# Optimization experiments

Measured on AMD Instinct MI355X. Metric: run time of the kernel, lower is better.

## Reference

```python
import jax, jax.numpy as jnp
import numpy as np

K = 20  # neighbors


def knn_idx(x, k):
    # x: [B, C, N]; returns indices of k nearest neighbors (incl. self): [B, N, k]
    xx = jnp.sum(x * x, axis=1)                          # [B, N]
    inner = jnp.einsum('bcn,bcm->bnm', x, x)             # [B, N, N]
    pd = 2.0 * inner - xx[:, :, None] - xx[:, None, :]   # -squared distance
    _, idx = jax.lax.top_k(pd, k)                        # [B, N, k]
    return idx


def graph_feature(x, k):
    # x: [B, C, N] -> edge features [B, 2C, N, k]
    idx = knn_idx(x, k)                                  # [B, N, k]
    xt = jnp.swapaxes(x, 1, 2)                           # [B, N, C]
    nbr = jax.vmap(lambda f, i: f[i])(xt, idx)           # [B, N, k, C]
    ctr = xt[:, :, None, :]                              # [B, N, 1, C]
    feat = jnp.concatenate(
        [nbr - ctr, jnp.broadcast_to(ctr, nbr.shape)], axis=-1)  # [B, N, k, 2C]
    return jnp.transpose(feat, (0, 3, 1, 2))             # [B, 2C, N, k]


def blk2(x, w, s, t):
    # 1x1 Conv2d (no bias) + folded BN + LeakyReLU(0.2); x: [B, C, N, k]
    y = jnp.einsum('oc,bcnk->bonk', w, x)
    y = y * s[None, :, None, None] + t[None, :, None, None]
    return jax.nn.leaky_relu(y, 0.2)


def blk1(x, w, s, t):
    # 1x1 Conv1d (no bias) + folded BN + LeakyReLU(0.2); x: [B, C, N]
    y = jnp.einsum('oc,bcn->bon', w, x)
    y = y * s[None, :, None] + t[None, :, None]
    return jax.nn.leaky_relu(y, 0.2)


def setup_inputs() -> dict:
    key = jax.random.key(0)
    ks = jax.random.split(key, 32)
    inp = {'x': jax.random.normal(ks[0], (16, 2, 2048), jnp.float32)}
    wdims = [(64, 4), (64, 64), (64, 128), (64, 64), (64, 128),
             (1024, 192), (512, 1216), (256, 512), (1, 256)]
    for i, (o, c) in enumerate(wdims):
        inp[f'w{i+1}'] = jax.random.normal(ks[1 + i], (o, c), jnp.float32) * np.float32((2.0 / c) ** 0.5)
    bdims = [64, 64, 64, 64, 64, 1024, 512, 256]
    for i, d in enumerate(bdims):
        inp[f's{i+1}'] = jax.random.uniform(ks[10 + i], (d,), jnp.float32, 0.5, 1.5)
        inp[f't{i+1}'] = jax.random.normal(ks[18 + i], (d,), jnp.float32) * 0.1
    return inp


def reference(x, w1, w2, w3, w4, w5, w6, w7, w8, w9,
              s1, s2, s3, s4, s5, s6, s7, s8,
              t1, t2, t3, t4, t5, t6, t7, t8):
    B, _, N = x.shape
    h = graph_feature(x, K)                 # [B, 4, N, k]
    h = blk2(h, w1, s1, t1)
    h = blk2(h, w2, s2, t2)
    x1 = jnp.max(h, axis=-1)                # [B, 64, N]
    h = graph_feature(x1, K)                # [B, 128, N, k]
    h = blk2(h, w3, s3, t3)
    h = blk2(h, w4, s4, t4)
    x2 = jnp.max(h, axis=-1)                # [B, 64, N]
    h = graph_feature(x2, K)                # [B, 128, N, k]
    h = blk2(h, w5, s5, t5)
    x3 = jnp.max(h, axis=-1)                # [B, 64, N]
    cat = jnp.concatenate([x1, x2, x3], axis=1)   # [B, 192, N]
    e = blk1(cat, w6, s6, t6)               # [B, 1024, N]
    g = jnp.max(e, axis=-1, keepdims=True)  # global max [B, 1024, 1]
    g = jnp.broadcast_to(g, (B, g.shape[1], N))
    h = jnp.concatenate([g, x1, x2, x3], axis=1)  # [B, 1216, N]
    h = blk1(h, w7, s7, t7)
    h = blk1(h, w8, s8, t8)                 # dropout = identity (eval)
    y = jnp.einsum('oc,bcn->bon', w9, h)    # [B, 1, N]
    return jax.nn.sigmoid(y.reshape(B, -1))
```

## Files before the change

kernel.cpp:

```cpp
#include <hip/hip_runtime.h>
#include <math.h>

#define KNNK 20
#define BEFORE(v1, g1, v2, g2) (((v1) > (v2)) || ((v1) == (v2) && (g1) < (g2)))

typedef unsigned short u16;
typedef unsigned int u32;
typedef unsigned long long u64;
typedef __attribute__((ext_vector_type(8))) short short8v;
typedef __attribute__((ext_vector_type(4))) float f32x4;

__device__ __forceinline__ float lrelu(float v) { return v >= 0.f ? v : 0.2f * v; }

__device__ __forceinline__ u16 f2bf(float v) {
    u32 u = __float_as_uint(v);
    u += 0x7fffu + ((u >> 16) & 1u);
    return (u16)(u >> 16);
}
__device__ __forceinline__ float bf2f(u16 h) { return __uint_as_float(((u32)h) << 16); }

__device__ __forceinline__ u32 ordf(float v) {
    u32 u = __float_as_uint(v);
    return u ^ ((u32)((int)u >> 31) | 0x80000000u);
}
__device__ __forceinline__ u64 mkkey(float v, int g) {
    return ((u64)ordf(v) << 32) | (u32)(~(u32)g);
}

__device__ __forceinline__ void cvt8(const float* __restrict__ p, short8v& H8, short8v& M8, short8v& L8) {
    float4 a = *(const float4*)(p);
    float4 b4 = *(const float4*)(p + 4);
    float v[8] = {a.x, a.y, a.z, a.w, b4.x, b4.y, b4.z, b4.w};
    short8v H, M, L;
#pragma unroll
    for (int i = 0; i < 8; ++i) {
        float x = v[i];
        u16 h = f2bf(x);
        float r1 = x - bf2f(h);
        u16 m = f2bf(r1);
        float r2 = r1 - bf2f(m);
        H[i] = (short)h;
        M[i] = (short)m;
        L[i] = (short)f2bf(r2);
    }
    H8 = H; M8 = M; L8 = L;
}

__global__ __launch_bounds__(256) void xx_kernel(const float* __restrict__ f, long bstride, int C,
                                                 float* __restrict__ xx) {
    int i = blockIdx.x * 256 + threadIdx.x;
    int b = i >> 11, n = i & 2047;
    const float* fb = f + (long)b * bstride;
    float s = 0.f;
    for (int c = 0; c < C; ++c) { float v = fb[c * 2048 + n]; s = fmaf(v, v, s); }
    xx[i] = s;
}

__device__ __forceinline__ void topk_row(const float* __restrict__ srow, int lane, int* __restrict__ orow) {
    float b1 = -INFINITY, b2 = -INFINITY, b3 = -INFINITY;
    int j1 = 0, j2 = 0, j3 = 0;
#pragma unroll
    for (int j = 0; j < 32; ++j) {
        float vv = srow[lane + 64 * j];
        bool c1 = vv > b1;
        bool c2 = vv > b2;
        bool c3 = vv > b3;
        b3 = c2 ? b2 : (c3 ? vv : b3);
        j3 = c2 ? j2 : (c3 ? j : j3);
        b2 = c1 ? b1 : (c2 ? vv : b2);
        j2 = c1 ? j1 : (c2 ? j : j2);
        b1 = c1 ? vv : b1;
        j1 = c1 ? j : j1;
    }

    u64 ka = mkkey(b1, lane + (j1 << 6));
#pragma unroll
    for (int size = 2; size <= 64; size <<= 1) {
#pragma unroll
        for (int stride = size >> 1; stride >= 1; stride >>= 1) {
            u64 ok = __shfl_xor(ka, stride);
            bool low = (lane & stride) == 0;
            bool asc = (lane & size) == 0;
            bool f = ka > ok;
            bool take = (low == asc) ? f : !f;
            ka = take ? ka : ok;
        }
    }
    u64 w19 = __shfl(ka, 19);
    unsigned used = (1u << j1) | (1u << j2) | (1u << j3);
    u64 pend = mkkey(b2, lane + (j2 << 6));
    int pstate = 0;
    while (__any(pend > w19)) {
        u64 act = __ballot(pend > w19);
        int L = __ffsll((long long)act) - 1;
        u64 ck = __shfl(pend, L);
        u64 cfb = __ballot(lane < 20 && ck > ka);
        int p = 20 - __popcll(cfb);
        u64 up = __shfl_up(ka, 1);
        if (lane < 20) {
            if (lane > p) ka = up;
            else if (lane == p) ka = ck;
        }
        if (lane == L) {
            if (pstate == 0) {
                pend = mkkey(b3, lane + (j3 << 6));
                pstate = 1;
            } else {
                float nb = -INFINITY;
                int nj = 0;
#pragma unroll
                for (int j = 0; j < 32; ++j) {
                    float vvv = ((used >> j) & 1u) ? -INFINITY : srow[lane + 64 * j];
                    if (vvv > nb) { nb = vvv; nj = j; }
                }
                used |= 1u << nj;
                pend = mkkey(nb, lane + (nj << 6));
            }
        }
        w19 = __shfl(ka, 19);
    }
    if (lane < KNNK) orow[lane] = (int)(~(u32)ka) & 2047;
}

__global__ __launch_bounds__(512, 4) void knn_kernel(const float* __restrict__ f, long bstride, int C,
                                                     const float* __restrict__ xx, int* __restrict__ idx_out) {
    __shared__ __align__(16) float lds[8 * 2048];
    int b = blockIdx.y;
    int n0 = blockIdx.x * 8;
    int t = threadIdx.x;
    const float* fb = f + (long)b * bstride;

    for (int e = t; e < C * 8; e += 512) {
        int c = e >> 3, j = e & 7;
        lds[e] = fb[c * 2048 + n0 + j];
    }
    __syncthreads();

    float acc[8][4];
#pragma unroll
    for (int i = 0; i < 8; ++i)
#pragma unroll
        for (int j = 0; j < 4; ++j) acc[i][j] = 0.f;
    int m0 = t * 4;
    for (int c = 0; c < C; ++c) {
        float4 b4 = *(const float4*)(fb + c * 2048 + m0);
        float bv[4] = {b4.x, b4.y, b4.z, b4.w};
        float4 a0 = *(const float4*)(lds + c * 8);
        float4 a1 = *(const float4*)(lds + c * 8 + 4);
        float av[8] = {a0.x, a0.y, a0.z, a0.w, a1.x, a1.y, a1.z, a1.w};
#pragma unroll
        for (int i = 0; i < 8; ++i)
#pragma unroll
            for (int j = 0; j < 4; ++j) acc[i][j] = fmaf(av[i], bv[j], acc[i][j]);
    }
    float xn[8];
#pragma unroll
    for (int i = 0; i < 8; ++i) xn[i] = xx[b * 2048 + n0 + i];
    float4 xm4 = *(const float4*)(xx + b * 2048 + m0);
    float xm[4] = {xm4.x, xm4.y, xm4.z, xm4.w};

    __syncthreads();
#pragma unroll
    for (int i = 0; i < 8; ++i) {
        float4 o;
        o.x = (2.f * acc[i][0] - xn[i]) - xm[0];
        o.y = (2.f * acc[i][1] - xn[i]) - xm[1];
        o.z = (2.f * acc[i][2] - xn[i]) - xm[2];
        o.w = (2.f * acc[i][3] - xn[i]) - xm[3];
        *(float4*)(lds + i * 2048 + m0) = o;
    }
    __syncthreads();

    int wave = t >> 6, lane = t & 63;
    topk_row(lds + wave * 2048, lane, idx_out + ((long)b * 2048 + n0 + wave) * KNNK);
}

__global__ __launch_bounds__(256) void pq_kernel(const float* __restrict__ f, long bstride, int C,
                                                 const float* __restrict__ W, float* __restrict__ P,
                                                 float* __restrict__ Q) {
    __shared__ __align__(16) float wa[64 * 64];
    __shared__ __align__(16) float wq[64 * 64];
    __shared__ __align__(16) float X[64 * 64];
    int b = blockIdx.y, n0 = blockIdx.x * 64, t = threadIdx.x;
    const float* fb = f + (long)b * bstride;
    for (int e = t; e < C * 64; e += 256) {
        int k = e >> 6, c = e & 63;
        float a = W[c * 2 * C + k];
        float bv = W[c * 2 * C + C + k];
        wa[k * 64 + c] = a;
        wq[k * 64 + c] = bv - a;
    }
    for (int e = t; e < C * 64; e += 256) {
        int k = e >> 6, j = e & 63;
        X[e] = fb[k * 2048 + n0 + j];
    }
    __syncthreads();
    int cg = t >> 4, ng = t & 15;
    float accP[4][4] = {}, accQ[4][4] = {};
    for (int k = 0; k < C; ++k) {
        float4 a4 = *(const float4*)(wa + k * 64 + cg * 4);
        float4 q4 = *(const float4*)(wq + k * 64 + cg * 4);
        float4 x4 = *(const float4*)(X + k * 64 + ng * 4);
        float av[4] = {a4.x, a4.y, a4.z, a4.w};
        float qv[4] = {q4.x, q4.y, q4.z, q4.w};
        float xv[4] = {x4.x, x4.y, x4.z, x4.w};
#pragma unroll
        for (int i = 0; i < 4; ++i)
#pragma unroll
            for (int j = 0; j < 4; ++j) {
                accP[i][j] = fmaf(av[i], xv[j], accP[i][j]);
                accQ[i][j] = fmaf(qv[i], xv[j], accQ[i][j]);
            }
    }
#pragma unroll
    for (int j = 0; j < 4; ++j) {
        long n = n0 + ng * 4 + j;
        float4 pv = {accP[0][j], accP[1][j], accP[2][j], accP[3][j]};
        float4 qv = {accQ[0][j], accQ[1][j], accQ[2][j], accQ[3][j]};
        *(float4*)(P + ((long)b * 2048 + n) * 64 + cg * 4) = pv;
        *(float4*)(Q + ((long)b * 2048 + n) * 64 + cg * 4) = qv;
    }
}

__global__ __launch_bounds__(256) void splitw3_kernel(const float* __restrict__ W, u16* __restrict__ h,
                                                      u16* __restrict__ m, u16* __restrict__ l) {
    int i = blockIdx.x * 256 + threadIdx.x;
    float v = W[i];
    u16 hh = f2bf(v);
    float r1 = v - bf2f(hh);
    u16 mm = f2bf(r1);
    float r2 = r1 - bf2f(mm);
    h[i] = hh;
    m[i] = mm;
    l[i] = f2bf(r2);
}

__global__ __launch_bounds__(256) void edge2_mfma_kernel(
    const float* __restrict__ P, const float* __restrict__ Q, const int* __restrict__ idx,
    const u16* __restrict__ Wh, const u16* __restrict__ Wm, const u16* __restrict__ Wl,
    const float* __restrict__ sa, const float* __restrict__ ta, const float* __restrict__ sb,
    const float* __restrict__ tb, float* __restrict__ out, int cofs) {
    __shared__ __align__(16) float h1t[192 * 68];
    __shared__ int idxl[160];
    int b = blockIdx.y, n0 = blockIdx.x * 8, t = threadIdx.x;
    if (t < 160) idxl[t] = idx[((long)b * 2048 + n0) * KNNK + t];
    __syncthreads();

    for (int it = t; it < 2560; it += 256) {
        int col = it % 160, cg = it / 160;
        int p = col / 20;
        int j = idxl[col];
        int n = n0 + p;
        float4 pv = *(const float4*)(P + ((long)b * 2048 + j) * 64 + cg * 4);
        float4 qv = *(const float4*)(Q + ((long)b * 2048 + n) * 64 + cg * 4);
        float4 sv = *(const float4*)(sa + cg * 4);
        float4 tv = *(const float4*)(ta + cg * 4);
        float4 o;
        o.x = lrelu(fmaf(sv.x, pv.x + qv.x, tv.x));
        o.y = lrelu(fmaf(sv.y, pv.y + qv.y, tv.y));
        o.z = lrelu(fmaf(sv.z, pv.z + qv.z, tv.z));
        o.w = lrelu(fmaf(sv.w, pv.w + qv.w, tv.w));
        *(float4*)(h1t + col * 68 + cg * 4) = o;
    }
    for (int it = t; it < 512; it += 256) {
        int col = 160 + (it & 31), cg = it >> 5;
        float4 z = {0.f, 0.f, 0.f, 0.f};
        *(float4*)(h1t + col * 68 + cg * 4) = z;
    }
    __syncthreads();

    int wave = t >> 6, lane = t & 63, l15 = lane & 15, lq = lane >> 4;
    f32x4 acc[3][4];
#pragma unroll
    for (int ct = 0; ct < 3; ++ct)
#pragma unroll
        for (int mt = 0; mt < 4; ++mt) {
            f32x4 z = {0.f, 0.f, 0.f, 0.f};
            acc[ct][mt] = z;
        }

#pragma unroll
    for (int ct = 0; ct < 3; ++ct) {
        int col = (wave * 3 + ct) * 16 + l15;
        short8v bh[2], bm[2], bl[2];
#pragma unroll
        for (int kh = 0; kh < 2; ++kh) cvt8(h1t + col * 68 + kh * 32 + lq * 8, bh[kh], bm[kh], bl[kh]);
#pragma unroll
        for (int mt = 0; mt < 4; ++mt) {
#pragma unroll
            for (int kh = 0; kh < 2; ++kh) {
                int wo = (mt * 16 + l15) * 64 + kh * 32 + lq * 8;
                short8v ah = *(const short8v*)(Wh + wo);
                short8v am = *(const short8v*)(Wm + wo);
                short8v al = *(const short8v*)(Wl + wo);
                acc[ct][mt] = __builtin_amdgcn_mfma_f32_16x16x32_bf16(ah, bh[kh], acc[ct][mt], 0, 0, 0);
                acc[ct][mt] = __builtin_amdgcn_mfma_f32_16x16x32_bf16(ah, bm[kh], acc[ct][mt], 0, 0, 0);
                acc[ct][mt] = __builtin_amdgcn_mfma_f32_16x16x32_bf16(am, bh[kh], acc[ct][mt], 0, 0, 0);
                acc[ct][mt] = __builtin_amdgcn_mfma_f32_16x16x32_bf16(am, bm[kh], acc[ct][mt], 0, 0, 0);
                acc[ct][mt] = __builtin_amdgcn_mfma_f32_16x16x32_bf16(ah, bl[kh], acc[ct][mt], 0, 0, 0);
                acc[ct][mt] = __builtin_amdgcn_mfma_f32_16x16x32_bf16(al, bh[kh], acc[ct][mt], 0, 0, 0);
            }
        }
    }
    __syncthreads();

#pragma unroll
    for (int ct = 0; ct < 3; ++ct) {
        int col = (wave * 3 + ct) * 16 + l15;
#pragma unroll
        for (int mt = 0; mt < 4; ++mt) {
            float4 d = {acc[ct][mt][0], acc[ct][mt][1], acc[ct][mt][2], acc[ct][mt][3]};
            *(float4*)(h1t + col * 68 + mt * 16 + lq * 4) = d;
        }
    }
    __syncthreads();

    for (int id = t; id < 512; id += 256) {
        int co = id & 63, p = id >> 6;
        float sv = sb[co], tv = tb[co];
        float m = -INFINITY;
#pragma unroll 4
        for (int kk = 0; kk < KNNK; ++kk)
            m = fmaxf(m, lrelu(fmaf(sv, h1t[(p * 20 + kk) * 68 + co], tv)));
        out[(long)b * (192 * 2048) + (long)(cofs + co) * 2048 + n0 + p] = m;
    }
}

__global__ __launch_bounds__(256) void edge2_kernel(
    const float* __restrict__ P, const float* __restrict__ Q, const int* __restrict__ idx,
    const float* __restrict__ W2, const float* __restrict__ sa, const float* __restrict__ ta,
    const float* __restrict__ sb, const float* __restrict__ tb, float* __restrict__ out, int cofs) {
    __shared__ __align__(16) float h1[64 * 164];
    __shared__ __align__(16) float w2l[64 * 64];
    __shared__ int idxl[160];
    int b = blockIdx.y, n0 = blockIdx.x * 8, t = threadIdx.x;
    if (t < 160) idxl[t] = idx[((long)b * 2048 + n0) * KNNK + t];
    for (int e = t; e < 4096; e += 256) { int co = e >> 6, ci = e & 63; w2l[ci * 64 + co] = W2[e]; }
    __syncthreads();
    for (int it = t; it < 2560; it += 256) {
        int col = it % 160, cg = it / 160;
        int p = col / 20;
        int j = idxl[col];
        int n = n0 + p;
        float4 pv = *(const float4*)(P + ((long)b * 2048 + j) * 64 + cg * 4);
        float4 qv = *(const float4*)(Q + ((long)b * 2048 + n) * 64 + cg * 4);
        float4 sv = *(const float4*)(sa + cg * 4);
        float4 tv = *(const float4*)(ta + cg * 4);
        h1[(cg * 4 + 0) * 164 + col] = lrelu(fmaf(sv.x, pv.x + qv.x, tv.x));
        h1[(cg * 4 + 1) * 164 + col] = lrelu(fmaf(sv.y, pv.y + qv.y, tv.y));
        h1[(cg * 4 + 2) * 164 + col] = lrelu(fmaf(sv.z, pv.z + qv.z, tv.z));
        h1[(cg * 4 + 3) * 164 + col] = lrelu(fmaf(sv.w, pv.w + qv.w, tv.w));
    }
    __syncthreads();
    int p = t & 7, co2 = t >> 3, c0 = co2 * 2;
    float acc0[20], acc1[20];
#pragma unroll
    for (int q = 0; q < 20; ++q) { acc0[q] = 0.f; acc1[q] = 0.f; }
#pragma unroll 4
    for (int k = 0; k < 64; ++k) {
        float2 w = *(const float2*)(w2l + k * 64 + c0);
        const float* hr = h1 + k * 164 + p * 20;
#pragma unroll
        for (int q = 0; q < 5; ++q) {
            float4 h4 = *(const float4*)(hr + q * 4);
            acc0[q * 4 + 0] = fmaf(w.x, h4.x, acc0[q * 4 + 0]);
            acc0[q * 4 + 1] = fmaf(w.x, h4.y, acc0[q * 4 + 1]);
            acc0[q * 4 + 2] = fmaf(w.x, h4.z, acc0[q * 4 + 2]);
            acc0[q * 4 + 3] = fmaf(w.x, h4.w, acc0[q * 4 + 3]);
            acc1[q * 4 + 0] = fmaf(w.y, h4.x, acc1[q * 4 + 0]);
            acc1[q * 4 + 1] = fmaf(w.y, h4.y, acc1[q * 4 + 1]);
            acc1[q * 4 + 2] = fmaf(w.y, h4.z, acc1[q * 4 + 2]);
            acc1[q * 4 + 3] = fmaf(w.y, h4.w, acc1[q * 4 + 3]);
        }
    }
    float s0 = sb[c0], t0v = tb[c0], s1 = sb[c0 + 1], t1v = tb[c0 + 1];
    float m0 = -INFINITY, m1 = -INFINITY;
#pragma unroll
    for (int q = 0; q < 20; ++q) {
        m0 = fmaxf(m0, lrelu(fmaf(s0, acc0[q], t0v)));
        m1 = fmaxf(m1, lrelu(fmaf(s1, acc1[q], t1v)));
    }
    out[(long)b * (192 * 2048) + (long)(cofs + c0) * 2048 + n0 + p] = m0;
    out[(long)b * (192 * 2048) + (long)(cofs + c0 + 1) * 2048 + n0 + p] = m1;
}

__global__ __launch_bounds__(256) void edge1_kernel(const float* __restrict__ P, const float* __restrict__ Q,
                                                    const int* __restrict__ idx, const float* __restrict__ s,
                                                    const float* __restrict__ tt, float* __restrict__ out,
                                                    int cofs) {
    __shared__ int idxl[80];
    int b = blockIdx.y, n0 = blockIdx.x * 4, t = threadIdx.x;
    int c = t & 63, p = t >> 6;
    if (t < 80) idxl[t] = idx[((long)b * 2048 + n0) * KNNK + t];
    __syncthreads();
    float qv = Q[((long)b * 2048 + n0 + p) * 64 + c];
    float sc = s[c], tc = tt[c];
    float m = -INFINITY;
    for (int kk = 0; kk < KNNK; ++kk) {
        int j = idxl[p * KNNK + kk];
        float v = P[((long)b * 2048 + j) * 64 + c];
        m = fmaxf(m, lrelu(fmaf(sc, v + qv, tc)));
    }
    out[(long)b * (192 * 2048) + (long)(cofs + c) * 2048 + n0 + p] = m;
}

__global__ __launch_bounds__(256) void gemm_kernel(
    const float* __restrict__ W, int ldw, int Kdim, const float* __restrict__ X, long xbstride,
    const float* __restrict__ s, const float* __restrict__ tvec, const float* __restrict__ bias, int M,
    float* __restrict__ out, long obstride, float* __restrict__ maxout) {
    __shared__ __align__(16) float wl[32 * 68];
    __shared__ __align__(16) float xl[32 * 132];
    int b = blockIdx.z, ct = blockIdx.x * 64, nt = blockIdx.y * 128, t = threadIdx.x;
    const float* Xb = X + (long)b * xbstride;
    int cg = t >> 4, ng = t & 15;
    float acc[4][8];
#pragma unroll
    for (int i = 0; i < 4; ++i)
#pragma unroll
        for (int j = 0; j < 8; ++j) acc[i][j] = 0.f;
    for (int k0 = 0; k0 < Kdim; k0 += 32) {
        __syncthreads();
        for (int e = t; e < 2048; e += 256) {
            int c = e >> 5, k = e & 31;
            wl[k * 68 + c] = W[(long)(ct + c) * ldw + k0 + k];
        }
        for (int e = t; e < 4096; e += 256) {
            int k = e >> 7, j = e & 127;
            xl[k * 132 + j] = Xb[(long)(k0 + k) * 2048 + nt + j];
        }
        __syncthreads();
#pragma unroll 8
        for (int k = 0; k < 32; ++k) {
            float4 w4 = *(const float4*)(wl + k * 68 + cg * 4);
            float4 xa = *(const float4*)(xl + k * 132 + ng * 4);
            float4 xb = *(const float4*)(xl + k * 132 + 64 + ng * 4);
            float wv[4] = {w4.x, w4.y, w4.z, w4.w};
            float xv[8] = {xa.x, xa.y, xa.z, xa.w, xb.x, xb.y, xb.z, xb.w};
#pragma unroll
            for (int i = 0; i < 4; ++i)
#pragma unroll
                for (int j = 0; j < 8; ++j) acc[i][j] = fmaf(wv[i], xv[j], acc[i][j]);
        }
    }
    if (maxout) {
        __syncthreads();
        float* scr = xl;
#pragma unroll
        for (int i = 0; i < 4; ++i) {
            int c = ct + cg * 4 + i;
            float sv = s[c], tv = tvec[c];
            float m = -INFINITY;
#pragma unroll
            for (int j = 0; j < 8; ++j) m = fmaxf(m, lrelu(fmaf(sv, acc[i][j], tv)));
            scr[(cg * 4 + i) * 16 + ng] = m;
        }
        __syncthreads();
        if (t < 64) {
            float m = scr[t * 16];
            for (int j = 1; j < 16; ++j) m = fmaxf(m, scr[t * 16 + j]);
            maxout[((long)b * M + ct + t) * 16 + blockIdx.y] = m;
        }
    } else {
#pragma unroll
        for (int i = 0; i < 4; ++i) {
            int c = ct + cg * 4 + i;
            float bv = bias ? bias[b * M + c] : 0.f;
            float sv = s[c], tv = tvec[c];
            float4 o0, o1;
            o0.x = lrelu(fmaf(sv, acc[i][0] + bv, tv));
            o0.y = lrelu(fmaf(sv, acc[i][1] + bv, tv));
            o0.z = lrelu(fmaf(sv, acc[i][2] + bv, tv));
            o0.w = lrelu(fmaf(sv, acc[i][3] + bv, tv));
            o1.x = lrelu(fmaf(sv, acc[i][4] + bv, tv));
            o1.y = lrelu(fmaf(sv, acc[i][5] + bv, tv));
            o1.z = lrelu(fmaf(sv, acc[i][6] + bv, tv));
            o1.w = lrelu(fmaf(sv, acc[i][7] + bv, tv));
            float* op = out + (long)b * obstride + (long)c * 2048 + nt + ng * 4;
            *(float4*)op = o0;
            *(float4*)(op + 64) = o1;
        }
    }
}

__global__ __launch_bounds__(256) void splitw_kernel(const float* __restrict__ W, int ldw, int koff, int K,
                                                     long total, u16* __restrict__ hi, u16* __restrict__ lo) {
    long i = (long)blockIdx.x * 256 + threadIdx.x;
    if (i >= total) return;
    long m = i / K, k = i - m * K;
    float v = W[m * ldw + koff + k];
    u16 h = f2bf(v);
    hi[i] = h;
    lo[i] = f2bf(v - bf2f(h));
}

__global__ __launch_bounds__(256) void splitx_kernel(const float* __restrict__ cat, u16* __restrict__ hi,
                                                     u16* __restrict__ lo) {
    __shared__ float lds[32][65];
    int b = blockIdx.y;
    int kt = blockIdx.x % 6, nt = blockIdx.x / 6;
    int k0 = kt * 32, n0 = nt * 64;
    int t = threadIdx.x;
#pragma unroll
    for (int i = 0; i < 8; ++i) {
        int e = t + i * 256;
        int k = e >> 6, n = e & 63;
        lds[k][n] = cat[(long)b * (192 * 2048) + (long)(k0 + k) * 2048 + n0 + n];
    }
    __syncthreads();
    int n = t >> 2, kq = t & 3;
    u16 hv[8], lv[8];
#pragma unroll
    for (int i = 0; i < 8; ++i) {
        float v = lds[kq * 8 + i][n];
        u16 h = f2bf(v);
        hv[i] = h;
        lv[i] = f2bf(v - bf2f(h));
    }
    long off = ((long)b * 2048 + n0 + n) * 192 + k0 + kq * 8;
    uint4 uh, ul;
    uh.x = (u32)hv[0] | ((u32)hv[1] << 16); uh.y = (u32)hv[2] | ((u32)hv[3] << 16);
    uh.z = (u32)hv[4] | ((u32)hv[5] << 16); uh.w = (u32)hv[6] | ((u32)hv[7] << 16);
    ul.x = (u32)lv[0] | ((u32)lv[1] << 16); ul.y = (u32)lv[2] | ((u32)lv[3] << 16);
    ul.z = (u32)lv[4] | ((u32)lv[5] << 16); ul.w = (u32)lv[6] | ((u32)lv[7] << 16);
    *(uint4*)(hi + off) = uh;
    *(uint4*)(lo + off) = ul;
}

template <int MT, int NT, bool MAXOUT>
__global__ __launch_bounds__(256, 2) void gemm_mfma(
    const u16* __restrict__ Whi, const u16* __restrict__ Wlo, const u16* __restrict__ Xhi,
    const u16* __restrict__ Xlo, int K, int M, const float* __restrict__ s,
    const float* __restrict__ tvec, const float* __restrict__ bias, float* __restrict__ outf,
    long obstride, u16* __restrict__ ohi, u16* __restrict__ olo, int oK, float* __restrict__ maxout) {
    constexpr int BM = MT * 32, BN = NT * 32;
    __shared__ __align__(16) u16 Ah[BM * 32], Al[BM * 32], Bh[BN * 32], Bl[BN * 32];
    __shared__ float scr[MAXOUT ? BM * 2 : 1];

    int b = blockIdx.z;
    int m0 = blockIdx.x * BM;
    int n0 = blockIdx.y * BN;
    int t = threadIdx.x;
    int wave = t >> 6, lane = t & 63;
    int wm = (wave >> 1) * (MT * 16);
    int wn = (wave & 1) * (NT * 16);
    const int l15 = lane & 15, lq = lane >> 4;
    const int kcs = lq ^ ((l15 >> 1) & 3);

    const u16* Xbh = Xhi + (long)b * 2048 * K;
    const u16* Xbl = Xlo + (long)b * 2048 * K;

    f32x4 zero4 = {0.f, 0.f, 0.f, 0.f};
    f32x4 acc[MT][NT];
#pragma unroll
    for (int i = 0; i < MT; ++i)
#pragma unroll
        for (int j = 0; j < NT; ++j) acc[i][j] = zero4;

    for (int k0 = 0; k0 < K; k0 += 32) {
        __syncthreads();
#pragma unroll
        for (int u = t; u < BM * 4; u += 256) {
            int row = u >> 2, kc = (u & 3) ^ ((row >> 1) & 3);
            long ga = (long)(m0 + row) * K + k0 + kc * 8;
            *(uint4*)(Ah + u * 8) = *(const uint4*)(Whi + ga);
            *(uint4*)(Al + u * 8) = *(const uint4*)(Wlo + ga);
        }
#pragma unroll
        for (int u = t; u < BN * 4; u += 256) {
            int row = u >> 2, kc = (u & 3) ^ ((row >> 1) & 3);
            long ga = (long)(n0 + row) * K + k0 + kc * 8;
            *(uint4*)(Bh + u * 8) = *(const uint4*)(Xbh + ga);
            *(uint4*)(Bl + u * 8) = *(const uint4*)(Xbl + ga);
        }
        __syncthreads();
        short8v a_h[MT], a_l[MT], b_h[NT], b_l[NT];
#pragma unroll
        for (int i = 0; i < MT; ++i) {
            int u = (wm + i * 16 + l15) * 4 + kcs;
            a_h[i] = *(const short8v*)(Ah + u * 8);
            a_l[i] = *(const short8v*)(Al + u * 8);
        }
#pragma unroll
        for (int j = 0; j < NT; ++j) {
            int u = (wn + j * 16 + l15) * 4 + kcs;
            b_h[j] = *(const short8v*)(Bh + u * 8);
            b_l[j] = *(const short8v*)(Bl + u * 8);
        }
#pragma unroll
        for (int i = 0; i < MT; ++i)
#pragma unroll
            for (int j = 0; j < NT; ++j) {
                acc[i][j] = __builtin_amdgcn_mfma_f32_16x16x32_bf16(a_h[i], b_h[j], acc[i][j], 0, 0, 0);
                acc[i][j] = __builtin_amdgcn_mfma_f32_16x16x32_bf16(a_h[i], b_l[j], acc[i][j], 0, 0, 0);
                acc[i][j] = __builtin_amdgcn_mfma_f32_16x16x32_bf16(a_l[i], b_h[j], acc[i][j], 0, 0, 0);
            }
    }

    if constexpr (MAXOUT) {
#pragma unroll
        for (int i = 0; i < MT; ++i)
#pragma unroll
            for (int r = 0; r < 4; ++r) {
                int ml = wm + i * 16 + lq * 4 + r;
                int c = m0 + ml;
                float sv = s[c], tv = tvec[c];
                float mx = -INFINITY;
#pragma unroll
                for (int j = 0; j < NT; ++j) mx = fmaxf(mx, lrelu(fmaf(sv, acc[i][j][r], tv)));
                mx = fmaxf(mx, __shfl_xor(mx, 1));
                mx = fmaxf(mx, __shfl_xor(mx, 2));
                mx = fmaxf(mx, __shfl_xor(mx, 4));
                mx = fmaxf(mx, __shfl_xor(mx, 8));
                if (l15 == 0) scr[ml * 2 + (wave & 1)] = mx;
            }
        __syncthreads();
        if (t < BM) maxout[((long)b * M + m0 + t) * 16 + blockIdx.y] = fmaxf(scr[t * 2], scr[t * 2 + 1]);
    } else if (outf) {
#pragma unroll
        for (int i = 0; i < MT; ++i)
#pragma unroll
            for (int r = 0; r < 4; ++r) {
                int c = m0 + wm + i * 16 + lq * 4 + r;
                float sv = s[c], tv = tvec[c];
                float bv = bias ? bias[b * M + c] : 0.f;
                float* op = outf + (long)b * obstride + (long)c * 2048 + n0 + wn;
#pragma unroll
                for (int j = 0; j < NT; ++j) op[j * 16 + l15] = lrelu(fmaf(sv, acc[i][j][r] + bv, tv));
            }
    } else {
#pragma unroll
        for (int i = 0; i < MT; ++i) {
            float sv[4], tv[4], bv[4];
#pragma unroll
            for (int r = 0; r < 4; ++r) {
                int c = m0 + wm + i * 16 + lq * 4 + r;
                sv[r] = s[c];
                tv[r] = tvec[c];
                bv[r] = bias ? bias[b * M + c] : 0.f;
            }
#pragma unroll
            for (int j = 0; j < NT; ++j) {
                long nb = ((long)b * 2048 + n0 + wn + j * 16 + l15) * oK + m0 + wm + i * 16 + lq * 4;
                ushort4 uh, ul;
                float v0 = lrelu(fmaf(sv[0], acc[i][j][0] + bv[0], tv[0]));
                float v1 = lrelu(fmaf(sv[1], acc[i][j][1] + bv[1], tv[1]));
                float v2 = lrelu(fmaf(sv[2], acc[i][j][2] + bv[2], tv[2]));
                float v3 = lrelu(fmaf(sv[3], acc[i][j][3] + bv[3], tv[3]));
                u16 h0 = f2bf(v0), h1 = f2bf(v1), h2 = f2bf(v2), h3 = f2bf(v3);
                uh.x = h0; uh.y = h1; uh.z = h2; uh.w = h3;
                ul.x = f2bf(v0 - bf2f(h0));
                ul.y = f2bf(v1 - bf2f(h1));
                ul.z = f2bf(v2 - bf2f(h2));
                ul.w = f2bf(v3 - bf2f(h3));
                *(ushort4*)(ohi + nb) = uh;
                *(ushort4*)(olo + nb) = ul;
            }
        }
    }
}

__global__ __launch_bounds__(256) void gmax_final(const float* __restrict__ ep, float* __restrict__ g) {
    int i = blockIdx.x * 256 + threadIdx.x;
    float m = ep[i * 16];
    for (int j = 1; j < 16; ++j) m = fmaxf(m, ep[i * 16 + j]);
    g[i] = m;
}

__global__ __launch_bounds__(64) void bias7_kernel(const float* __restrict__ w7, const float* __restrict__ g,
                                                   float* __restrict__ bias7) {
    int o = blockIdx.x;
    int b = o >> 9, co = o & 511;
    int lane = threadIdx.x;
    float acc = 0.f;
    for (int j = lane; j < 1024; j += 64) acc = fmaf(w7[(long)co * 1216 + j], g[b * 1024 + j], acc);
#pragma unroll
    for (int off = 32; off >= 1; off >>= 1) acc += __shfl_xor(acc, off);
    if (lane == 0) bias7[o] = acc;
}

__global__ __launch_bounds__(256) void w9_kernel(const float* __restrict__ w9, const float* __restrict__ h8,
                                                 float* __restrict__ out) {
    int i = blockIdx.x * 256 + threadIdx.x;
    int b = i >> 11, n = i & 2047;
    const float* hb = h8 + (long)b * 256 * 2048 + n;
    float acc = 0.f;
    for (int c = 0; c < 256; ++c) acc = fmaf(w9[c], hb[c * 2048], acc);
    out[i] = 1.f / (1.f + expf(-acc));
}

extern "C" void kernel_launch(void* const* d_in, const int* in_sizes, int n_in,
                              void* d_out, int out_size, void* d_ws, size_t ws_size,
                              hipStream_t stream) {
    (void)in_sizes; (void)n_in; (void)out_size;
    const float* x  = (const float*)d_in[0];
    const float* w1 = (const float*)d_in[1];
    const float* w2 = (const float*)d_in[2];
    const float* w3 = (const float*)d_in[3];
    const float* w4 = (const float*)d_in[4];
    const float* w5 = (const float*)d_in[5];
    const float* w6 = (const float*)d_in[6];
    const float* w7 = (const float*)d_in[7];
    const float* w8 = (const float*)d_in[8];
    const float* w9 = (const float*)d_in[9];
    const float* s1 = (const float*)d_in[10]; const float* t1 = (const float*)d_in[11];
    const float* s2 = (const float*)d_in[12]; const float* t2 = (const float*)d_in[13];
    const float* s3 = (const float*)d_in[14]; const float* t3 = (const float*)d_in[15];
    const float* s4 = (const float*)d_in[16]; const float* t4 = (const float*)d_in[17];
    const float* s5 = (const float*)d_in[18]; const float* t5 = (const float*)d_in[19];
    const float* s6 = (const float*)d_in[20]; const float* t6 = (const float*)d_in[21];
    const float* s7 = (const float*)d_in[22]; const float* t7 = (const float*)d_in[23];
    const float* s8 = (const float*)d_in[24]; const float* t8 = (const float*)d_in[25];

    float* cat = (float*)d_ws;
    float* xxb = cat + (long)6291456;
    int* idxb = (int*)(xxb + 32768);
    float* ep = (float*)(idxb + 655360);
    float* g  = ep + 262144;
    float* b7 = g + 16384;
    float* h8 = b7 + 8192;
    float* P  = h8 + 8388608;
    float* Q  = P + 2097152;
    u16* h7hi = (u16*)(Q + 2097152);
    u16* h7lo = h7hi + 16777216;
    u16* cathi = h7lo + 16777216;
    u16* catlo = cathi + 6291456;
    u16* w6h = catlo + 6291456;
    u16* w6l = w6h + 196608;
    u16* w7h = w6l + 196608;
    u16* w7l = w7h + 98304;
    u16* w8h = w7l + 98304;
    u16* w8l = w8h + 131072;
    const size_t NEED = 173375488;
    bool big = ws_size >= NEED;

    u16* w2L = h7hi;
    u16* w4L = h7hi + 12288;

    dim3 blk(256);
    dim3 blk512(512);
    long catstride = 192 * 2048;

    if (big) {
        splitw3_kernel<<<16, blk, 0, stream>>>(w2, w2L, w2L + 4096, w2L + 8192);
        splitw3_kernel<<<16, blk, 0, stream>>>(w4, w4L, w4L + 4096, w4L + 8192);
    }

    xx_kernel<<<128, blk, 0, stream>>>(x, 2 * 2048, 2, xxb);
    knn_kernel<<<dim3(256, 16), blk512, 0, stream>>>(x, 2 * 2048, 2, xxb, idxb);
    pq_kernel<<<dim3(32, 16), blk, 0, stream>>>(x, 2 * 2048, 2, w1, P, Q);
    if (big)
        edge2_mfma_kernel<<<dim3(256, 16), blk, 0, stream>>>(P, Q, idxb, w2L, w2L + 4096, w2L + 8192,
                                                             s1, t1, s2, t2, cat, 0);
    else
        edge2_kernel<<<dim3(256, 16), blk, 0, stream>>>(P, Q, idxb, w2, s1, t1, s2, t2, cat, 0);
    xx_kernel<<<128, blk, 0, stream>>>(cat, catstride, 64, xxb);
    knn_kernel<<<dim3(256, 16), blk512, 0, stream>>>(cat, catstride, 64, xxb, idxb);
    pq_kernel<<<dim3(32, 16), blk, 0, stream>>>(cat, catstride, 64, w3, P, Q);
    if (big)
        edge2_mfma_kernel<<<dim3(256, 16), blk, 0, stream>>>(P, Q, idxb, w4L, w4L + 4096, w4L + 8192,
                                                             s3, t3, s4, t4, cat, 64);
    else
        edge2_kernel<<<dim3(256, 16), blk, 0, stream>>>(P, Q, idxb, w4, s3, t3, s4, t4, cat, 64);
    xx_kernel<<<128, blk, 0, stream>>>(cat + 64 * 2048, catstride, 64, xxb);
    knn_kernel<<<dim3(256, 16), blk512, 0, stream>>>(cat + 64 * 2048, catstride, 64, xxb, idxb);
    pq_kernel<<<dim3(32, 16), blk, 0, stream>>>(cat + 64 * 2048, catstride, 64, w5, P, Q);
    edge1_kernel<<<dim3(512, 16), blk, 0, stream>>>(P, Q, idxb, s5, t5, cat, 128);

    if (big) {
        splitw_kernel<<<768, blk, 0, stream>>>(w6, 192, 0, 192, 196608, w6h, w6l);
        splitw_kernel<<<384, blk, 0, stream>>>(w7, 1216, 1024, 192, 98304, w7h, w7l);
        splitw_kernel<<<512, blk, 0, stream>>>(w8, 512, 0, 512, 131072, w8h, w8l);
        splitx_kernel<<<dim3(192, 16), blk, 0, stream>>>(cat, cathi, catlo);
        gemm_mfma<4, 4, true><<<dim3(8, 16, 16), blk, 0, stream>>>(
            w6h, w6l, cathi, catlo, 192, 1024, s6, t6, nullptr, nullptr, 0, nullptr, nullptr, 0, ep);
        gmax_final<<<64, blk, 0, stream>>>(ep, g);
        bias7_kernel<<<dim3(16 * 512), dim3(64), 0, stream>>>(w7, g, b7);
        gemm_mfma<4, 4, false><<<dim3(4, 16, 16), blk, 0, stream>>>(
            w7h, w7l, cathi, catlo, 192, 512, s7, t7, b7, nullptr, 0, h7hi, h7lo, 512, nullptr);
        gemm_mfma<2, 4, false><<<dim3(4, 16, 16), blk, 0, stream>>>(
            w8h, w8l, h7hi, h7lo, 512, 256, s8, t8, nullptr, h8, (long)256 * 2048, nullptr, nullptr, 0,
            nullptr);
        w9_kernel<<<128, blk, 0, stream>>>(w9, h8, (float*)d_out);
    } else {
        float* h7f = (float*)h7hi;
        gemm_kernel<<<dim3(16, 16, 16), blk, 0, stream>>>(w6, 192, 192, cat, catstride, s6, t6, nullptr,
                                                          1024, nullptr, 0, ep);
        gmax_final<<<64, blk, 0, stream>>>(ep, g);
        bias7_kernel<<<dim3(16 * 512), dim3(64), 0, stream>>>(w7, g, b7);
        gemm_kernel<<<dim3(8, 16, 16), blk, 0, stream>>>(w7 + 1024, 1216, 192, cat, catstride, s7, t7, b7,
                                                         512, h7f, (long)512 * 2048, nullptr);
        gemm_kernel<<<dim3(4, 16, 16), blk, 0, stream>>>(w8, 512, 512, h7f, (long)512 * 2048, s8, t8,
                                                         nullptr, 256, h8, (long)256 * 2048, nullptr);
        w9_kernel<<<128, blk, 0, stream>>>(w9, h8, (float*)d_out);
    }
}
```

Baseline: 1.042 ms.

## Split kNN top-k into two half-row passes to halve LDS and raise occupancy

The kNN kernel now stages only half of each distance row (1024 columns) in shared memory at a time. It computes a top-20 for each half and merges the two sorted lists with a wave-wide bitonic sort, which roughly halves the LDS footprint so launch bounds can allow 8 blocks per CU instead of 4. The cost is an extra barrier phase, a second bitonic sort, and a merge step per row. The occupancy target also puts pressure on registers, given the 32-float accumulator tile.

```diff
diff --git a/kernel.cpp b/kernel.cpp
--- a/kernel.cpp
+++ b/kernel.cpp
@@ -2,7 +2,6 @@
 #include <math.h>
 
 #define KNNK 20
-#define BEFORE(v1, g1, v2, g2) (((v1) > (v2)) || ((v1) == (v2) && (g1) < (g2)))
 
 typedef unsigned short u16;
 typedef unsigned int u32;
@@ -56,11 +55,11 @@
     xx[i] = s;
 }
 
-__device__ __forceinline__ void topk_row(const float* __restrict__ srow, int lane, int* __restrict__ orow) {
+__device__ __forceinline__ u64 topk20_half(const float* __restrict__ srow, int lane, int colbase) {
     float b1 = -INFINITY, b2 = -INFINITY, b3 = -INFINITY;
     int j1 = 0, j2 = 0, j3 = 0;
 #pragma unroll
-    for (int j = 0; j < 32; ++j) {
+    for (int j = 0; j < 16; ++j) {
         float vv = srow[lane + 64 * j];
         bool c1 = vv > b1;
         bool c2 = vv > b2;
@@ -72,8 +71,7 @@
         b1 = c1 ? vv : b1;
         j1 = c1 ? j : j1;
     }
-
-    u64 ka = mkkey(b1, lane + (j1 << 6));
+    u64 ka = mkkey(b1, colbase + lane + (j1 << 6));
 #pragma unroll
     for (int size = 2; size <= 64; size <<= 1) {
 #pragma unroll
@@ -88,7 +86,7 @@
     }
     u64 w19 = __shfl(ka, 19);
     unsigned used = (1u << j1) | (1u << j2) | (1u << j3);
-    u64 pend = mkkey(b2, lane + (j2 << 6));
+    u64 pend = mkkey(b2, colbase + lane + (j2 << 6));
     int pstate = 0;
     while (__any(pend > w19)) {
         u64 act = __ballot(pend > w19);
@@ -103,28 +101,47 @@
         }
         if (lane == L) {
             if (pstate == 0) {
-                pend = mkkey(b3, lane + (j3 << 6));
+                pend = mkkey(b3, colbase + lane + (j3 << 6));
                 pstate = 1;
             } else {
                 float nb = -INFINITY;
                 int nj = 0;
 #pragma unroll
-                for (int j = 0; j < 32; ++j) {
+                for (int j = 0; j < 16; ++j) {
                     float vvv = ((used >> j) & 1u) ? -INFINITY : srow[lane + 64 * j];
                     if (vvv > nb) { nb = vvv; nj = j; }
                 }
                 used |= 1u << nj;
-                pend = mkkey(nb, lane + (nj << 6));
+                pend = mkkey(nb, colbase + lane + (nj << 6));
             }
         }
         w19 = __shfl(ka, 19);
     }
-    if (lane < KNNK) orow[lane] = (int)(~(u32)ka) & 2047;
-}
-
-__global__ __launch_bounds__(512, 4) void knn_kernel(const float* __restrict__ f, long bstride, int C,
+    return ka;
+}
+
+__device__ __forceinline__ u64 merge20(u64 kA, u64 kB, int lane) {
+    u64 kb = __shfl(kB, (lane - 20) & 63);
+    u64 ka = lane < 20 ? kA : (lane < 40 ? kb : 0ULL);
+#pragma unroll
+    for (int size = 2; size <= 64; size <<= 1) {
+#pragma unroll
+        for (int stride = size >> 1; stride >= 1; stride >>= 1) {
+            u64 ok = __shfl_xor(ka, stride);
+            bool low = (lane & stride) == 0;
+            bool asc = (lane & size) == 0;
+            bool f = ka > ok;
+            bool take = (low == asc) ? f : !f;
+            ka = take ? ka : ok;
+        }
+    }
+    return ka;
+}
+
+__global__ __launch_bounds__(512, 8) void knn_kernel(const float* __restrict__ f, long bstride, int C,
                                                      const float* __restrict__ xx, int* __restrict__ idx_out) {
-    __shared__ __align__(16) float lds[8 * 2048];
+    __shared__ __align__(16) float pd[8 * 1028];
+    __shared__ __align__(16) float Asm[64 * 8];
     int b = blockIdx.y;
     int n0 = blockIdx.x * 8;
     int t = threadIdx.x;
@@ -132,7 +149,7 @@
 
     for (int e = t; e < C * 8; e += 512) {
         int c = e >> 3, j = e & 7;
-        lds[e] = fb[c * 2048 + n0 + j];
+        Asm[e] = fb[c * 2048 + n0 + j];
     }
     __syncthreads();
 
@@ -145,8 +162,9 @@
     for (int c = 0; c < C; ++c) {
         float4 b4 = *(const float4*)(fb + c * 2048 + m0);
         float bv[4] = {b4.x, b4.y, b4.z, b4.w};
-        float4 a0 = *(const float4*)(lds + c * 8);
-        float4 a1 = *(const float4*)(lds + c * 8 + 4);
+        const float* ar = Asm + c * 8;
+        float4 a0 = *(const float4*)(ar);
+        float4 a1 = *(const float4*)(ar + 4);
         float av[8] = {a0.x, a0.y, a0.z, a0.w, a1.x, a1.y, a1.z, a1.w};
 #pragma unroll
         for (int i = 0; i < 8; ++i)
@@ -159,20 +177,40 @@
     float4 xm4 = *(const float4*)(xx + b * 2048 + m0);
     float xm[4] = {xm4.x, xm4.y, xm4.z, xm4.w};
 
-    __syncthreads();
-#pragma unroll
-    for (int i = 0; i < 8; ++i) {
-        float4 o;
-        o.x = (2.f * acc[i][0] - xn[i]) - xm[0];
-        o.y = (2.f * acc[i][1] - xn[i]) - xm[1];
-        o.z = (2.f * acc[i][2] - xn[i]) - xm[2];
-        o.w = (2.f * acc[i][3] - xn[i]) - xm[3];
-        *(float4*)(lds + i * 2048 + m0) = o;
-    }
-    __syncthreads();
-
     int wave = t >> 6, lane = t & 63;
-    topk_row(lds + wave * 2048, lane, idx_out + ((long)b * 2048 + n0 + wave) * KNNK);
+
+    if (m0 < 1024) {
+#pragma unroll
+        for (int i = 0; i < 8; ++i) {
+            float4 o;
+            o.x = (2.f * acc[i][0] - xn[i]) - xm[0];
+            o.y = (2.f * acc[i][1] - xn[i]) - xm[1];
+            o.z = (2.f * acc[i][2] - xn[i]) - xm[2];
+            o.w = (2.f * acc[i][3] - xn[i]) - xm[3];
+            *(float4*)(pd + i * 1028 + m0) = o;
+        }
+    }
+    __syncthreads();
+    u64 kA = topk20_half(pd + wave * 1028, lane, 0);
+    __syncthreads();
+
+    if (m0 >= 1024) {
+        int lc = m0 - 1024;
+#pragma unroll
+        for (int i = 0; i < 8; ++i) {
+            float4 o;
+            o.x = (2.f * acc[i][0] - xn[i]) - xm[0];
+            o.y = (2.f * acc[i][1] - xn[i]) - xm[1];
+            o.z = (2.f * acc[i][2] - xn[i]) - xm[2];
+            o.w = (2.f * acc[i][3] - xn[i]) - xm[3];
+            *(float4*)(pd + i * 1028 + lc) = o;
+        }
+    }
+    __syncthreads();
+    u64 kB = topk20_half(pd + wave * 1028, lane, 1024);
+
+    u64 fk = merge20(kA, kB, lane);
+    if (lane < KNNK) idx_out[((long)b * 2048 + n0 + wave) * KNNK + lane] = (int)(~(u32)fk) & 2047;
 }
 
 __global__ __launch_bounds__(256) void pq_kernel(const float* __restrict__ f, long bstride, int C,
```

Result: slower. 1.169 ms (+12.1%).
